# Kernel tuning notes

Hardware: AMD Instinct MI355X
Metric: run time of the kernel (lower is better)

## Reference

```python
import jax, jax.numpy as jnp
import numpy as np

N = 50000
E = 1600000
F_IN = 4
F_OUT = 32
PERIODS = 12


def setup_inputs() -> dict:
    key = jax.random.key(0)
    ks = jax.random.split(key, 18)
    s_in = 1.0 / np.sqrt(F_IN)
    s_cat = 1.0 / np.sqrt(2 * F_OUT)
    s_out = 1.0 / np.sqrt(F_OUT)
    inp = {
        'x': jax.random.normal(ks[0], (N, F_IN, PERIODS), dtype=jnp.float32),
        'edge_index': jax.random.randint(ks[1], (2, E), 0, N, dtype=jnp.int32),
        'attention': jax.random.uniform(ks[2], (PERIODS,), dtype=jnp.float32),
        # GRU update gate z: GCNConv weight/bias + Linear(2*F_OUT -> F_OUT)
        'Wz': jax.random.normal(ks[3], (F_IN, F_OUT), jnp.float32) * s_in,
        'bz': jnp.zeros((F_OUT,), jnp.float32),
        'Lz': jax.random.normal(ks[4], (2 * F_OUT, F_OUT), jnp.float32) * s_cat,
        'lz': jnp.zeros((F_OUT,), jnp.float32),
        # reset gate r
        'Wr': jax.random.normal(ks[5], (F_IN, F_OUT), jnp.float32) * s_in,
        'br': jnp.zeros((F_OUT,), jnp.float32),
        'Lr': jax.random.normal(ks[6], (2 * F_OUT, F_OUT), jnp.float32) * s_cat,
        'lr': jnp.zeros((F_OUT,), jnp.float32),
        # candidate h
        'Wh': jax.random.normal(ks[7], (F_IN, F_OUT), jnp.float32) * s_in,
        'bh': jnp.zeros((F_OUT,), jnp.float32),
        'Lh': jax.random.normal(ks[8], (2 * F_OUT, F_OUT), jnp.float32) * s_cat,
        'lh': jnp.zeros((F_OUT,), jnp.float32),
        # outer Linear(32 -> periods)
        'Wo': jax.random.normal(ks[9], (F_OUT, PERIODS), jnp.float32) * s_out,
        'bo': jnp.zeros((PERIODS,), jnp.float32),
    }
    return inp


def reference(x, edge_index, attention, Wz, bz, Lz, lz, Wr, br, Lr, lr, Wh, bh, Lh, lh, Wo, bo):
    n = x.shape[0]
    # gcn_norm: add self loops, symmetric D^-1/2 (A+I) D^-1/2
    loop = jnp.arange(n, dtype=edge_index.dtype)
    row = jnp.concatenate([edge_index[0], loop])  # source
    col = jnp.concatenate([edge_index[1], loop])  # target
    w = jnp.ones(row.shape[0], dtype=x.dtype)
    deg = jax.ops.segment_sum(w, col, num_segments=n)
    dinv = jnp.where(deg > 0, jax.lax.rsqrt(deg), 0.0)
    norm = dinv[row] * dinv[col]  # [E+N]

    def conv(xt, W, b):
        h = xt @ W                                   # [N, F_OUT]
        msg = h[row] * norm[:, None]                 # gather + scale
        return jax.ops.segment_sum(msg, col, num_segments=n) + b

    H0 = jnp.zeros((n, F_OUT), dtype=x.dtype)  # A3TGCN passes H=None each period

    def tgcn(xt):
        Z = jax.nn.sigmoid(jnp.concatenate([conv(xt, Wz, bz), H0], axis=1) @ Lz + lz)
        R = jax.nn.sigmoid(jnp.concatenate([conv(xt, Wr, br), H0], axis=1) @ Lr + lr)
        Ht = jnp.tanh(jnp.concatenate([conv(xt, Wh, bh), H0 * R], axis=1) @ Lh + lh)
        return Z * H0 + (1.0 - Z) * Ht

    Hs = jax.vmap(tgcn)(jnp.moveaxis(x, 2, 0))       # [T, N, F_OUT]
    probs = jax.nn.softmax(attention)
    H = jnp.einsum('tnc,t->nc', Hs, probs)           # attention-weighted sum over periods
    return jax.nn.relu(H) @ Wo + bo                  # [N, PERIODS]
```

## Files before the change

### kernel.cpp

```cpp
#include <hip/hip_runtime.h>
#include <hip/hip_fp16.h>
#include <math.h>

#define CHUNK 6400
#define CAPG  5120
#define BKN   128
#define FXS 4096.0f
#define FXI 2.44140625e-4f

__global__ void k_pre(const float* __restrict__ Wz, const float* __restrict__ Lz, const float* __restrict__ lz,
                      const float* __restrict__ Wh, const float* __restrict__ Lh, const float* __restrict__ lh,
                      const float* __restrict__ bz, const float* __restrict__ bh,
                      const float* __restrict__ att,
                      float* __restrict__ AzT, float* __restrict__ AhT,
                      float* __restrict__ bzp, float* __restrict__ bhp, float* __restrict__ probs,
                      int* __restrict__ gcur) {
  int t = threadIdx.x;
  gcur[t] = 0; gcur[t + 256] = 0;
  if (t < 128) {
    int f = t >> 2, k = t & 3;
    float s = 0.f, s2 = 0.f;
    for (int j = 0; j < 32; ++j) {
      s  = fmaf(Wz[k * 32 + j], Lz[j * 32 + f], s);
      s2 = fmaf(Wh[k * 32 + j], Lh[j * 32 + f], s2);
    }
    AzT[t] = s; AhT[t] = s2;
  }
  if (t >= 128 && t < 160) {
    int f = t - 128;
    float s = lz[f], s2 = lh[f];
    for (int j = 0; j < 32; ++j) {
      s  = fmaf(bz[j], Lz[j * 32 + f], s);
      s2 = fmaf(bh[j], Lh[j * 32 + f], s2);
    }
    bzp[f] = s; bhp[f] = s2;
  }
  if (t == 160) {
    float m = att[0];
    for (int i = 1; i < 12; ++i) m = fmaxf(m, att[i]);
    float e[12]; float s = 0.f;
    for (int i = 0; i < 12; ++i) { e[i] = __expf(att[i] - m); s += e[i]; }
    for (int i = 0; i < 12; ++i) probs[i] = e[i] / s;
  }
}

__global__ __launch_bounds__(1024) void k_part(const int* __restrict__ row, const int* __restrict__ col,
                                               int E, int nbkt,
                                               int* __restrict__ gcur, unsigned* __restrict__ part) {
  __shared__ unsigned spak[CHUNK];
  __shared__ unsigned short sbkt[CHUNK];
  __shared__ unsigned char slc[CHUNK];
  __shared__ int hist[512], sscan[512], scur[512], gbase[512];
  int t = threadIdx.x;
  int base = blockIdx.x * CHUNK;
  int cnt = E - base; if (cnt > CHUNK) cnt = CHUNK;
  if (t < 512) hist[t] = 0;
  __syncthreads();
  for (int i = t; i < cnt; i += 1024) {
    int c = col[base + i];
    int b = c >> 7;
    sbkt[i] = (unsigned short)b;
    slc[i]  = (unsigned char)(c & 127);
    atomicAdd(&hist[b], 1);
  }
  __syncthreads();
  int v = 0;
  if (t < 512) { v = hist[t]; sscan[t] = v; }
  __syncthreads();
  for (int off = 1; off < 512; off <<= 1) {
    int a = 0;
    if (t < 512 && t >= off) a = sscan[t - off];
    __syncthreads();
    if (t < 512) sscan[t] += a;
    __syncthreads();
  }
  if (t < 512) {
    sscan[t] -= v;
    gbase[t] = (v > 0) ? atomicAdd(&gcur[t], v) : 0;
    scur[t] = 0;
  }
  __syncthreads();
  for (int i = t; i < cnt; i += 1024) {
    int r = row[base + i];
    int b = sbkt[i];
    int pos = atomicAdd(&scur[b], 1);
    spak[sscan[b] + pos] = ((unsigned)r << 7) | (unsigned)slc[i];
  }
  __syncthreads();
  int hw = t >> 5, l32 = t & 31;
  for (int b = hw; b < nbkt; b += 32) {
    int len = hist[b], gb = gbase[b], src = sscan[b];
    int lim = CAPG - gb; if (lim > len) lim = len;
    unsigned* dst = part + (size_t)b * CAPG + gb;
    for (int j = l32; j < lim; j += 32) dst[j] = spak[src + j];
  }
}

__global__ __launch_bounds__(1024) void k_deg_xh(const unsigned* __restrict__ part, const int* __restrict__ gcur,
                                                 const float4* __restrict__ x4,
                                                 float* __restrict__ dinv, uint2* __restrict__ xq, int n) {
  __shared__ int hist[BKN];
  __shared__ float sdi[BKN];
  int b = blockIdx.x, t = threadIdx.x;
  int cnt = gcur[b]; if (cnt > CAPG) cnt = CAPG;
  const unsigned* src = part + (size_t)b * CAPG;
  if (t < BKN) hist[t] = 0;
  __syncthreads();
  for (int i = t; i < cnt; i += 1024) atomicAdd(&hist[src[i] & 127u], 1);
  __syncthreads();
  if (t < BKN) {
    int node = b * BKN + t;
    float di = rsqrtf((float)(hist[t] + 1));
    sdi[t] = di;
    if (node < n) dinv[node] = di;
  }
  __syncthreads();
  int gb = b * (BKN * 12);
  for (int j = t; j < BKN * 12; j += 1024) {
    int gi = gb + j;
    if (gi < n * 12) {
      float4 f = x4[gi];
      float d = sdi[j / 12] * FXS;
      int a0 = __float2int_rn(d * f.x), a1 = __float2int_rn(d * f.y);
      int a2 = __float2int_rn(d * f.z), a3 = __float2int_rn(d * f.w);
      uint2 u;
      u.x = ((unsigned)a0 & 0xffffu) | ((unsigned)a1 << 16);
      u.y = ((unsigned)a2 & 0xffffu) | ((unsigned)a3 << 16);
      xq[gi] = u;
    }
  }
}

__global__ __launch_bounds__(1024) void k_acc(const unsigned* __restrict__ part, const int* __restrict__ gcur,
                                              const float* __restrict__ dinv, const uint4* __restrict__ xq4,
                                              const float* __restrict__ AzT, const float* __restrict__ AhT,
                                              const float* __restrict__ bzp, const float* __restrict__ bhp,
                                              const float* __restrict__ probs,
                                              const float* __restrict__ Wo, const float* __restrict__ bo,
                                              float* __restrict__ out, int n) {
  __shared__ int sAcc[BKN * 49];
  __shared__ float sdi[BKN];
  __shared__ float4 sAz4[32], sAh4[32];
  __shared__ float sbzp[32], sbhp[32], sprobs[12], sbo[12], sWo[384];
  int t = threadIdx.x;
  int b = blockIdx.x;
  int nb = b * BKN;

  if (t < 32) {
    sAz4[t] = ((const float4*)AzT)[t];
    sAh4[t] = ((const float4*)AhT)[t];
    sbzp[t] = bzp[t]; sbhp[t] = bhp[t];
  }
  if (t >= 32 && t < 44) { sprobs[t - 32] = probs[t - 32]; sbo[t - 32] = bo[t - 32]; }
  if (t >= 64 && t < 448) sWo[t - 64] = Wo[t - 64];
  if (t >= 512 && t < 512 + BKN) {
    int node = nb + t - 512;
    sdi[t - 512] = (node < n) ? dinv[node] : 0.f;
  }
  if (t < BKN * 6) {
    int ln = t / 6, cc = t - (t / 6) * 6;
    int node = nb + ln;
    int* ap = sAcc + ln * 49 + cc * 8;
    if (node < n) {
      uint4 v = xq4[(unsigned)node * 6u + cc];
      ap[0] = (int)(short)v.x; ap[1] = (int)v.x >> 16;
      ap[2] = (int)(short)v.y; ap[3] = (int)v.y >> 16;
      ap[4] = (int)(short)v.z; ap[5] = (int)v.z >> 16;
      ap[6] = (int)(short)v.w; ap[7] = (int)v.w >> 16;
    } else {
      ap[0] = 0; ap[1] = 0; ap[2] = 0; ap[3] = 0;
      ap[4] = 0; ap[5] = 0; ap[6] = 0; ap[7] = 0;
    }
  }
  __syncthreads();

  int cnt = gcur[b]; if (cnt > CAPG) cnt = CAPG;
  const unsigned* src = part + (size_t)b * CAPG;
  const int NG = 170;
  int g = t / 6, c = t - (t / 6) * 6;
#define PROC(e) { \
    uint4 v = xq4[((e) >> 7) * 6u + (unsigned)c]; \
    int* ap = sAcc + (int)((e) & 127u) * 49 + c * 8; \
    atomicAdd(ap + 0, (int)(short)v.x); atomicAdd(ap + 1, (int)v.x >> 16); \
    atomicAdd(ap + 2, (int)(short)v.y); atomicAdd(ap + 3, (int)v.y >> 16); \
    atomicAdd(ap + 4, (int)(short)v.z); atomicAdd(ap + 5, (int)v.z >> 16); \
    atomicAdd(ap + 6, (int)(short)v.w); atomicAdd(ap + 7, (int)v.w >> 16); \
  }
  if (g < NG) {
    int i = g;
    for (; i + 3 * NG < cnt; i += 4 * NG) {
      unsigned e0 = src[i], e1 = src[i + NG], e2 = src[i + 2 * NG], e3 = src[i + 3 * NG];
      PROC(e0) PROC(e1) PROC(e2) PROC(e3)
    }
    for (; i < cnt; i += NG) { unsigned e = src[i]; PROC(e) }
  }
#undef PROC
  __syncthreads();

  float* sF = (float*)sAcc;
  for (int k = t; k < BKN * 48; k += 1024) {
    int ln = k / 48, m = k - ln * 48;
    int idx = ln * 49 + m;
    int raw = sAcc[idx];
    sF[idx] = (float)raw * (sdi[ln] * FXI);
  }
  __syncthreads();

  for (int k = 0; k < 4; ++k) {
    int u = t + k * 1024;
    int ln = u >> 5, f = u & 31;
    bool valid = (nb + ln < n);
    const float* y = sF + ln * 49;
    float4 az = sAz4[f], ah = sAh4[f];
    float bzf = sbzp[f], bhf = sbhp[f];
    float acc2 = 0.f;
#pragma unroll
    for (int tt = 0; tt < 12; ++tt) {
      float y0 = y[tt], y1 = y[12 + tt], y2 = y[24 + tt], y3 = y[36 + tt];
      float za = fmaf(az.x, y0, fmaf(az.y, y1, fmaf(az.z, y2, fmaf(az.w, y3, bzf))));
      float ha = fmaf(ah.x, y0, fmaf(ah.y, y1, fmaf(ah.z, y2, fmaf(ah.w, y3, bhf))));
      float ez = __expf(za);
      float ax = fabsf(ha);
      float e2 = __expf(-2.f * ax);
      float gg = (1.f - e2) / ((1.f + ez) * (1.f + e2));
      acc2 = fmaf(sprobs[tt], copysignf(gg, ha), acc2);
    }
    __syncthreads();
    if (valid) sF[ln * 49 + f] = fmaxf(acc2, 0.f);
  }
  __syncthreads();

  for (int k = 0; k < 2; ++k) {
    int u = t + k * 1024;
    if (u < BKN * 12) {
      int ln = u / 12, p = u - (u / 12) * 12;
      int node = nb + ln;
      if (node < n) {
        float s = sbo[p];
        const float* h = sF + ln * 49;
        const float* wv = sWo + p;
#pragma unroll
        for (int f2 = 0; f2 < 32; ++f2) s = fmaf(h[f2], wv[f2 * 12], s);
        out[node * 12 + p] = s;
      }
    }
  }
}

extern "C" void kernel_launch(void* const* d_in, const int* in_sizes, int n_in,
                              void* d_out, int out_size, void* d_ws, size_t ws_size,
                              hipStream_t stream) {
  const float* x   = (const float*)d_in[0];
  const int*   ei  = (const int*)d_in[1];
  const float* att = (const float*)d_in[2];
  const float* Wz  = (const float*)d_in[3];
  const float* bz  = (const float*)d_in[4];
  const float* Lz  = (const float*)d_in[5];
  const float* lz  = (const float*)d_in[6];
  const float* Wh  = (const float*)d_in[11];
  const float* bh  = (const float*)d_in[12];
  const float* Lh  = (const float*)d_in[13];
  const float* lh  = (const float*)d_in[14];
  const float* Wo  = (const float*)d_in[15];
  const float* bo  = (const float*)d_in[16];
  float* out = (float*)d_out;

  const int N = in_sizes[0] / (4 * 12);
  const int E = in_sizes[1] / 2;
  const int NBKT = (N + BKN - 1) / BKN;
  const int* row = ei;
  const int* col = ei + E;

  char* w = (char*)d_ws;
  size_t o = 0;
  auto alloc = [&](size_t bytes) -> char* {
    o = (o + 255) & ~(size_t)255;
    char* p = w + o; o += bytes; return p;
  };
  float* pAzT   = (float*)alloc(128 * 4);
  float* pAhT   = (float*)alloc(128 * 4);
  float* pbzp   = (float*)alloc(32 * 4);
  float* pbhp   = (float*)alloc(32 * 4);
  float* pprobs = (float*)alloc(12 * 4);
  int*   pgcur  = (int*)alloc(512 * 4);
  float* pdinv  = (float*)alloc((size_t)NBKT * BKN * 4);
  unsigned* ppart = (unsigned*)alloc((size_t)512 * CAPG * 4);
  uint2* pxq    = (uint2*)alloc((size_t)NBKT * BKN * 12 * 8);
  (void)ws_size; (void)n_in; (void)out_size;

  k_pre<<<1, 256, 0, stream>>>(Wz, Lz, lz, Wh, Lh, lh, bz, bh, att,
                               pAzT, pAhT, pbzp, pbhp, pprobs, pgcur);
  k_part<<<(E + CHUNK - 1) / CHUNK, 1024, 0, stream>>>(row, col, E, NBKT, pgcur, ppart);
  k_deg_xh<<<NBKT, 1024, 0, stream>>>(ppart, pgcur, (const float4*)x, pdinv, pxq, N);
  k_acc<<<NBKT, 1024, 0, stream>>>(ppart, pgcur, pdinv, (const uint4*)pxq,
                                   pAzT, pAhT, pbzp, pbhp, pprobs,
                                   Wo, bo, out, N);
}
```

Measured before the change: 174.6 us.

## Use smaller destination buckets and compute degrees with global atomics during partitioning

Bucket size drops from 128 to 50 nodes, giving 1000 buckets, each accumulated by a 512-thread block. That spreads the scatter-accumulate over many more blocks and lowers shared-memory use per block. Degree counting moves out of a separate per-bucket histogram pass and into global atomics inside the partition kernel. The quantize kernel becomes a flat elementwise pass, and the degree array is zeroed in the setup kernel. The cost is extra global atomic traffic and more bins to scan in the partition kernel.

```diff
diff --git a/kernel.cpp b/kernel.cpp
--- a/kernel.cpp
+++ b/kernel.cpp
@@ -3,20 +3,24 @@
 #include <math.h>
 
 #define CHUNK 6400
-#define CAPG  5120
-#define BKN   128
+#define BK    50
+#define NBIN  1024
+#define CAPG  1920
 #define FXS 4096.0f
 #define FXI 2.44140625e-4f
 
-__global__ void k_pre(const float* __restrict__ Wz, const float* __restrict__ Lz, const float* __restrict__ lz,
+__global__ __launch_bounds__(1024) void k_pre(const float* __restrict__ Wz, const float* __restrict__ Lz, const float* __restrict__ lz,
                       const float* __restrict__ Wh, const float* __restrict__ Lh, const float* __restrict__ lh,
                       const float* __restrict__ bz, const float* __restrict__ bh,
                       const float* __restrict__ att,
                       float* __restrict__ AzT, float* __restrict__ AhT,
                       float* __restrict__ bzp, float* __restrict__ bhp, float* __restrict__ probs,
-                      int* __restrict__ gcur) {
+                      int* __restrict__ gcur, int* __restrict__ deg, int n) {
   int t = threadIdx.x;
-  gcur[t] = 0; gcur[t + 256] = 0;
+  int gid = blockIdx.x * 1024 + t;
+  if (gid < n) deg[gid] = 0;
+  if (blockIdx.x != 0) return;
+  gcur[t] = 0;
   if (t < 128) {
     int f = t >> 2, k = t & 3;
     float s = 0.f, s2 = 0.f;
@@ -46,118 +50,95 @@
 
 __global__ __launch_bounds__(1024) void k_part(const int* __restrict__ row, const int* __restrict__ col,
                                                int E, int nbkt,
-                                               int* __restrict__ gcur, unsigned* __restrict__ part) {
+                                               int* __restrict__ gcur, int* __restrict__ deg,
+                                               unsigned* __restrict__ part) {
   __shared__ unsigned spak[CHUNK];
-  __shared__ unsigned short sbkt[CHUNK];
-  __shared__ unsigned char slc[CHUNK];
-  __shared__ int hist[512], sscan[512], scur[512], gbase[512];
+  __shared__ int hist[NBIN], sscan[NBIN], scur[NBIN], gbase[NBIN];
   int t = threadIdx.x;
   int base = blockIdx.x * CHUNK;
   int cnt = E - base; if (cnt > CHUNK) cnt = CHUNK;
-  if (t < 512) hist[t] = 0;
+  hist[t] = 0;
   __syncthreads();
   for (int i = t; i < cnt; i += 1024) {
     int c = col[base + i];
-    int b = c >> 7;
-    sbkt[i] = (unsigned short)b;
-    slc[i]  = (unsigned char)(c & 127);
-    atomicAdd(&hist[b], 1);
-  }
-  __syncthreads();
-  int v = 0;
-  if (t < 512) { v = hist[t]; sscan[t] = v; }
-  __syncthreads();
-  for (int off = 1; off < 512; off <<= 1) {
+    atomicAdd(&hist[c / BK], 1);
+    atomicAdd(&deg[c], 1);
+  }
+  __syncthreads();
+  int v = hist[t];
+  sscan[t] = v;
+  __syncthreads();
+  for (int off = 1; off < NBIN; off <<= 1) {
     int a = 0;
-    if (t < 512 && t >= off) a = sscan[t - off];
+    if (t >= off) a = sscan[t - off];
     __syncthreads();
-    if (t < 512) sscan[t] += a;
+    sscan[t] += a;
     __syncthreads();
   }
-  if (t < 512) {
-    sscan[t] -= v;
-    gbase[t] = (v > 0) ? atomicAdd(&gcur[t], v) : 0;
-    scur[t] = 0;
-  }
+  sscan[t] -= v;
+  gbase[t] = (v > 0) ? atomicAdd(&gcur[t], v) : 0;
+  scur[t] = 0;
   __syncthreads();
   for (int i = t; i < cnt; i += 1024) {
+    int c = col[base + i];
     int r = row[base + i];
-    int b = sbkt[i];
+    int b = c / BK, lc = c - b * BK;
     int pos = atomicAdd(&scur[b], 1);
-    spak[sscan[b] + pos] = ((unsigned)r << 7) | (unsigned)slc[i];
-  }
-  __syncthreads();
-  int hw = t >> 5, l32 = t & 31;
-  for (int b = hw; b < nbkt; b += 32) {
+    spak[sscan[b] + pos] = ((unsigned)r << 6) | (unsigned)lc;
+  }
+  __syncthreads();
+  int grp = t >> 3, l8 = t & 7;
+  for (int b = grp; b < nbkt; b += 128) {
     int len = hist[b], gb = gbase[b], src = sscan[b];
     int lim = CAPG - gb; if (lim > len) lim = len;
     unsigned* dst = part + (size_t)b * CAPG + gb;
-    for (int j = l32; j < lim; j += 32) dst[j] = spak[src + j];
-  }
-}
-
-__global__ __launch_bounds__(1024) void k_deg_xh(const unsigned* __restrict__ part, const int* __restrict__ gcur,
-                                                 const float4* __restrict__ x4,
-                                                 float* __restrict__ dinv, uint2* __restrict__ xq, int n) {
-  __shared__ int hist[BKN];
-  __shared__ float sdi[BKN];
-  int b = blockIdx.x, t = threadIdx.x;
-  int cnt = gcur[b]; if (cnt > CAPG) cnt = CAPG;
-  const unsigned* src = part + (size_t)b * CAPG;
-  if (t < BKN) hist[t] = 0;
-  __syncthreads();
-  for (int i = t; i < cnt; i += 1024) atomicAdd(&hist[src[i] & 127u], 1);
-  __syncthreads();
-  if (t < BKN) {
-    int node = b * BKN + t;
-    float di = rsqrtf((float)(hist[t] + 1));
-    sdi[t] = di;
-    if (node < n) dinv[node] = di;
-  }
-  __syncthreads();
-  int gb = b * (BKN * 12);
-  for (int j = t; j < BKN * 12; j += 1024) {
-    int gi = gb + j;
-    if (gi < n * 12) {
-      float4 f = x4[gi];
-      float d = sdi[j / 12] * FXS;
-      int a0 = __float2int_rn(d * f.x), a1 = __float2int_rn(d * f.y);
-      int a2 = __float2int_rn(d * f.z), a3 = __float2int_rn(d * f.w);
-      uint2 u;
-      u.x = ((unsigned)a0 & 0xffffu) | ((unsigned)a1 << 16);
-      u.y = ((unsigned)a2 & 0xffffu) | ((unsigned)a3 << 16);
-      xq[gi] = u;
-    }
-  }
-}
-
-__global__ __launch_bounds__(1024) void k_acc(const unsigned* __restrict__ part, const int* __restrict__ gcur,
-                                              const float* __restrict__ dinv, const uint4* __restrict__ xq4,
-                                              const float* __restrict__ AzT, const float* __restrict__ AhT,
-                                              const float* __restrict__ bzp, const float* __restrict__ bhp,
-                                              const float* __restrict__ probs,
-                                              const float* __restrict__ Wo, const float* __restrict__ bo,
-                                              float* __restrict__ out, int n) {
-  __shared__ int sAcc[BKN * 49];
-  __shared__ float sdi[BKN];
+    for (int j = l8; j < lim; j += 8) dst[j] = spak[src + j];
+  }
+}
+
+__global__ __launch_bounds__(1024) void k_dx(const float4* __restrict__ x4, const int* __restrict__ deg,
+                                             uint2* __restrict__ xq, int n12) {
+  int gid = blockIdx.x * 1024 + threadIdx.x;
+  if (gid < n12) {
+    float d = rsqrtf((float)(deg[gid / 12] + 1)) * FXS;
+    float4 f = x4[gid];
+    int a0 = __float2int_rn(d * f.x), a1 = __float2int_rn(d * f.y);
+    int a2 = __float2int_rn(d * f.z), a3 = __float2int_rn(d * f.w);
+    uint2 u;
+    u.x = ((unsigned)a0 & 0xffffu) | ((unsigned)a1 << 16);
+    u.y = ((unsigned)a2 & 0xffffu) | ((unsigned)a3 << 16);
+    xq[gid] = u;
+  }
+}
+
+__global__ __launch_bounds__(512) void k_acc(const unsigned* __restrict__ part, const int* __restrict__ gcur,
+                                             const int* __restrict__ deg, const uint4* __restrict__ xq4,
+                                             const float* __restrict__ AzT, const float* __restrict__ AhT,
+                                             const float* __restrict__ bzp, const float* __restrict__ bhp,
+                                             const float* __restrict__ probs,
+                                             const float* __restrict__ Wo, const float* __restrict__ bo,
+                                             float* __restrict__ out, int n) {
+  __shared__ int sAcc[BK * 49];
+  __shared__ float sdi[BK];
   __shared__ float4 sAz4[32], sAh4[32];
   __shared__ float sbzp[32], sbhp[32], sprobs[12], sbo[12], sWo[384];
   int t = threadIdx.x;
   int b = blockIdx.x;
-  int nb = b * BKN;
+  int nb = b * BK;
 
   if (t < 32) {
     sAz4[t] = ((const float4*)AzT)[t];
     sAh4[t] = ((const float4*)AhT)[t];
     sbzp[t] = bzp[t]; sbhp[t] = bhp[t];
-  }
-  if (t >= 32 && t < 44) { sprobs[t - 32] = probs[t - 32]; sbo[t - 32] = bo[t - 32]; }
+  } else if (t < 44) {
+    sprobs[t - 32] = probs[t - 32]; sbo[t - 32] = bo[t - 32];
+  }
   if (t >= 64 && t < 448) sWo[t - 64] = Wo[t - 64];
-  if (t >= 512 && t < 512 + BKN) {
-    int node = nb + t - 512;
-    sdi[t - 512] = (node < n) ? dinv[node] : 0.f;
-  }
-  if (t < BKN * 6) {
+  if (t >= 448 && t < 448 + BK) {
+    int node = nb + t - 448;
+    sdi[t - 448] = (node < n) ? rsqrtf((float)(deg[node] + 1)) : 0.f;
+  }
+  if (t < BK * 6) {
     int ln = t / 6, cc = t - (t / 6) * 6;
     int node = nb + ln;
     int* ap = sAcc + ln * 49 + cc * 8;
@@ -176,11 +157,11 @@
 
   int cnt = gcur[b]; if (cnt > CAPG) cnt = CAPG;
   const unsigned* src = part + (size_t)b * CAPG;
-  const int NG = 170;
+  const int NG = 85;
   int g = t / 6, c = t - (t / 6) * 6;
 #define PROC(e) { \
-    uint4 v = xq4[((e) >> 7) * 6u + (unsigned)c]; \
-    int* ap = sAcc + (int)((e) & 127u) * 49 + c * 8; \
+    uint4 v = xq4[((e) >> 6) * 6u + (unsigned)c]; \
+    int* ap = sAcc + (int)((e) & 63u) * 49 + c * 8; \
     atomicAdd(ap + 0, (int)(short)v.x); atomicAdd(ap + 1, (int)v.x >> 16); \
     atomicAdd(ap + 2, (int)(short)v.y); atomicAdd(ap + 3, (int)v.y >> 16); \
     atomicAdd(ap + 4, (int)(short)v.z); atomicAdd(ap + 5, (int)v.z >> 16); \
@@ -198,7 +179,7 @@
   __syncthreads();
 
   float* sF = (float*)sAcc;
-  for (int k = t; k < BKN * 48; k += 1024) {
+  for (int k = t; k < BK * 48; k += 512) {
     int ln = k / 48, m = k - ln * 48;
     int idx = ln * 49 + m;
     int raw = sAcc[idx];
@@ -207,32 +188,34 @@
   __syncthreads();
 
   for (int k = 0; k < 4; ++k) {
-    int u = t + k * 1024;
+    int u = t + k * 512;
     int ln = u >> 5, f = u & 31;
-    bool valid = (nb + ln < n);
-    const float* y = sF + ln * 49;
-    float4 az = sAz4[f], ah = sAh4[f];
-    float bzf = sbzp[f], bhf = sbhp[f];
+    bool act = (u < BK * 32) && (nb + ln < n);
     float acc2 = 0.f;
+    if (act) {
+      const float* y = sF + ln * 49;
+      float4 az = sAz4[f], ah = sAh4[f];
+      float bzf = sbzp[f], bhf = sbhp[f];
 #pragma unroll
-    for (int tt = 0; tt < 12; ++tt) {
-      float y0 = y[tt], y1 = y[12 + tt], y2 = y[24 + tt], y3 = y[36 + tt];
-      float za = fmaf(az.x, y0, fmaf(az.y, y1, fmaf(az.z, y2, fmaf(az.w, y3, bzf))));
-      float ha = fmaf(ah.x, y0, fmaf(ah.y, y1, fmaf(ah.z, y2, fmaf(ah.w, y3, bhf))));
-      float ez = __expf(za);
-      float ax = fabsf(ha);
-      float e2 = __expf(-2.f * ax);
-      float gg = (1.f - e2) / ((1.f + ez) * (1.f + e2));
-      acc2 = fmaf(sprobs[tt], copysignf(gg, ha), acc2);
+      for (int tt = 0; tt < 12; ++tt) {
+        float y0 = y[tt], y1 = y[12 + tt], y2 = y[24 + tt], y3 = y[36 + tt];
+        float za = fmaf(az.x, y0, fmaf(az.y, y1, fmaf(az.z, y2, fmaf(az.w, y3, bzf))));
+        float ha = fmaf(ah.x, y0, fmaf(ah.y, y1, fmaf(ah.z, y2, fmaf(ah.w, y3, bhf))));
+        float ez = __expf(za);
+        float ax = fabsf(ha);
+        float e2 = __expf(-2.f * ax);
+        float gg = (1.f - e2) / ((1.f + ez) * (1.f + e2));
+        acc2 = fmaf(sprobs[tt], copysignf(gg, ha), acc2);
+      }
     }
     __syncthreads();
-    if (valid) sF[ln * 49 + f] = fmaxf(acc2, 0.f);
+    if (act) sF[ln * 49 + f] = fmaxf(acc2, 0.f);
   }
   __syncthreads();
 
   for (int k = 0; k < 2; ++k) {
-    int u = t + k * 1024;
-    if (u < BKN * 12) {
+    int u = t + k * 512;
+    if (u < BK * 12) {
       int ln = u / 12, p = u - (u / 12) * 12;
       int node = nb + ln;
       if (node < n) {
@@ -267,7 +250,7 @@
 
   const int N = in_sizes[0] / (4 * 12);
   const int E = in_sizes[1] / 2;
-  const int NBKT = (N + BKN - 1) / BKN;
+  const int NBKT = (N + BK - 1) / BK;
   const int* row = ei;
   const int* col = ei + E;
 
@@ -282,17 +265,17 @@
   float* pbzp   = (float*)alloc(32 * 4);
   float* pbhp   = (float*)alloc(32 * 4);
   float* pprobs = (float*)alloc(12 * 4);
-  int*   pgcur  = (int*)alloc(512 * 4);
-  float* pdinv  = (float*)alloc((size_t)NBKT * BKN * 4);
-  unsigned* ppart = (unsigned*)alloc((size_t)512 * CAPG * 4);
-  uint2* pxq    = (uint2*)alloc((size_t)NBKT * BKN * 12 * 8);
+  int*   pgcur  = (int*)alloc(NBIN * 4);
+  int*   pdeg   = (int*)alloc((size_t)N * 4);
+  unsigned* ppart = (unsigned*)alloc((size_t)NBIN * CAPG * 4);
+  uint2* pxq    = (uint2*)alloc((size_t)N * 12 * 8);
   (void)ws_size; (void)n_in; (void)out_size;
 
-  k_pre<<<1, 256, 0, stream>>>(Wz, Lz, lz, Wh, Lh, lh, bz, bh, att,
-                               pAzT, pAhT, pbzp, pbhp, pprobs, pgcur);
-  k_part<<<(E + CHUNK - 1) / CHUNK, 1024, 0, stream>>>(row, col, E, NBKT, pgcur, ppart);
-  k_deg_xh<<<NBKT, 1024, 0, stream>>>(ppart, pgcur, (const float4*)x, pdinv, pxq, N);
-  k_acc<<<NBKT, 1024, 0, stream>>>(ppart, pgcur, pdinv, (const uint4*)pxq,
-                                   pAzT, pAhT, pbzp, pbhp, pprobs,
-                                   Wo, bo, out, N);
-}
+  k_pre<<<(N + 1023) / 1024, 1024, 0, stream>>>(Wz, Lz, lz, Wh, Lh, lh, bz, bh, att,
+                                                pAzT, pAhT, pbzp, pbhp, pprobs, pgcur, pdeg, N);
+  k_part<<<(E + CHUNK - 1) / CHUNK, 1024, 0, stream>>>(row, col, E, NBKT, pgcur, pdeg, ppart);
+  k_dx<<<(N * 12 + 1023) / 1024, 1024, 0, stream>>>((const float4*)x, pdeg, pxq, N * 12);
+  k_acc<<<NBKT, 512, 0, stream>>>(ppart, pgcur, pdeg, (const uint4*)pxq,
+                                  pAzT, pAhT, pbzp, pbhp, pprobs,
+                                  Wo, bo, out, N);
+}
```

Result: slower. 220.5 us (+26.3%).
